# Optimization experiments

Hardware: AMD Instinct MI355X
Metric: run time of the kernel (lower is better)

Reference implementation:

```python
import jax, jax.numpy as jnp
from jax import lax
import numpy as np

B, T, D, H, O, L = 64, 1024, 256, 512, 256, 2


def setup_inputs() -> dict:
    key = jax.random.key(0)
    ks = jax.random.split(key, 12)
    s_in = 1.0 / np.sqrt(H)
    inp = {
        "x": jax.random.normal(ks[0], (B, T, D), dtype=jnp.float32),
        "W_ih0": jax.random.uniform(ks[1], (H, D), jnp.float32, -s_in, s_in),
        "W_hh0": jax.random.uniform(ks[2], (H, H), jnp.float32, -s_in, s_in),
        "b_ih0": jax.random.uniform(ks[3], (H,), jnp.float32, -s_in, s_in),
        "b_hh0": jax.random.uniform(ks[4], (H,), jnp.float32, -s_in, s_in),
        "W_ih1": jax.random.uniform(ks[5], (H, H), jnp.float32, -s_in, s_in),
        "W_hh1": jax.random.uniform(ks[6], (H, H), jnp.float32, -s_in, s_in),
        "b_ih1": jax.random.uniform(ks[7], (H,), jnp.float32, -s_in, s_in),
        "b_hh1": jax.random.uniform(ks[8], (H,), jnp.float32, -s_in, s_in),
        "W_fc": jax.random.uniform(ks[9], (O, H), jnp.float32, -s_in, s_in),
        "b_fc": jax.random.uniform(ks[10], (O,), jnp.float32, -s_in, s_in),
    }
    return inp


def _rnn_layer(inp, W_ih, W_hh, b_ih, b_hh):
    # inp: [B, T, Din] -> outputs [B, T, H], final hidden [B, H]
    # PyTorch: h_t = tanh(x_t @ W_ih^T + b_ih + h_{t-1} @ W_hh^T + b_hh)
    xW = jnp.einsum("btd,hd->bth", inp, W_ih) + b_ih + b_hh  # precompute input proj

    def step(h, xw_t):
        h = jnp.tanh(xw_t + h @ W_hh.T)
        return h, h

    h0 = jnp.zeros((inp.shape[0], W_hh.shape[0]), dtype=inp.dtype)
    hT, hs = lax.scan(step, h0, jnp.swapaxes(xW, 0, 1))  # scan over time
    return jnp.swapaxes(hs, 0, 1), hT


def reference(x, W_ih0, W_hh0, b_ih0, b_hh0, W_ih1, W_hh1, b_ih1, b_hh1, W_fc, b_fc):
    out0, _ = _rnn_layer(x, W_ih0, W_hh0, b_ih0, b_hh0)
    _, hT1 = _rnn_layer(out0, W_ih1, W_hh1, b_ih1, b_hh1)
    # fc applied to hn[-1] (last layer final hidden state)
    return hT1 @ W_fc.T + b_fc  # [B, O]
```

## Files before the change

kernel.cpp:

```cpp
#include <hip/hip_runtime.h>
#include <cmath>


#define Bdim 64
#define Tdim 1024
#define Ddim 256
#define Hdim 512
#define Odim 256

template <int K>
__global__ __launch_bounds__(1024) void gemm_rows(const float* A, const float* W,
                                                  const float* __restrict__ bias_a,
                                                  const float* __restrict__ bias_b,
                                                  float* C) {
  constexpr int KT = 16;
  __shared__ __align__(16) float As[64][KT];
  __shared__ __align__(16) float Ws[KT][516];
  const int t = threadIdx.x;
  const size_t row0 = (size_t)blockIdx.x * 64;
  const int tn = t & 127;
  const int tm = t >> 7;

  float acc[8][4];
#pragma unroll
  for (int i = 0; i < 8; ++i)
#pragma unroll
    for (int j = 0; j < 4; ++j) acc[i][j] = 0.f;

  const int r_st = t >> 4;
  const int k_st = t & 15;

  for (int k0 = 0; k0 < K; k0 += KT) {
    As[r_st][k_st] = A[(row0 + r_st) * K + k0 + k_st];
#pragma unroll
    for (int rep = 0; rep < 8; ++rep) {
      const int idx = rep * 1024 + t;
      const int n = idx >> 4;
      const int kk = idx & 15;
      Ws[kk][n] = W[(size_t)n * K + k0 + kk];
    }
    __syncthreads();
#pragma unroll
    for (int kk = 0; kk < KT; ++kk) {
      float a[8];
#pragma unroll
      for (int i = 0; i < 8; ++i) a[i] = As[tm * 8 + i][kk];
      const float4 w = *(const float4*)&Ws[kk][tn * 4];
#pragma unroll
      for (int i = 0; i < 8; ++i) {
        acc[i][0] = fmaf(a[i], w.x, acc[i][0]);
        acc[i][1] = fmaf(a[i], w.y, acc[i][1]);
        acc[i][2] = fmaf(a[i], w.z, acc[i][2]);
        acc[i][3] = fmaf(a[i], w.w, acc[i][3]);
      }
    }
    __syncthreads();
  }
  float bn[4];
#pragma unroll
  for (int j = 0; j < 4; ++j) bn[j] = bias_a[tn * 4 + j] + bias_b[tn * 4 + j];
#pragma unroll
  for (int i = 0; i < 8; ++i) {
    float4 v;
    v.x = acc[i][0] + bn[0];
    v.y = acc[i][1] + bn[1];
    v.z = acc[i][2] + bn[2];
    v.w = acc[i][3] + bn[3];
    *(float4*)&C[(row0 + tm * 8 + i) * (size_t)Hdim + tn * 4] = v;
  }
}

__global__ __launch_bounds__(512, 2) void rnn_scan_coop(
    float* xw,
    const float* __restrict__ Whh,
    unsigned long long* hbuf,
    float* h_final,
    const int store_seq) {
  const int bi = blockIdx.x;
  const int b = bi & 63;
  const int q = bi >> 6;
  const int t = threadIdx.x;
  const int ks = t >> 6;
  const int jp = t & 63;
  const int jl0 = jp * 2;
  const int jg0 = q * 128 + jl0;

  __shared__ __align__(16) float h_s[Hdim];
  __shared__ __align__(16) float red[8][128];

  float4 W0[16], W1[16];
  {
    const float4* w0p = (const float4*)(Whh + (size_t)jg0 * Hdim + ks * 64);
    const float4* w1p = (const float4*)(Whh + (size_t)(jg0 + 1) * Hdim + ks * 64);
#pragma unroll
    for (int c = 0; c < 16; ++c) {
      W0[c] = w0p[c];
      W1[c] = w1p[c];
    }
  }
#pragma unroll
  for (int c = 0; c < 16; ++c) {
    asm volatile("" : "+v"(W0[c].x), "+v"(W0[c].y), "+v"(W0[c].z), "+v"(W0[c].w));
    asm volatile("" : "+v"(W1[c].x), "+v"(W1[c].y), "+v"(W1[c].z), "+v"(W1[c].w));
  }

  h_s[t] = 0.0f;
  __syncthreads();

  float* row = xw + (size_t)b * Tdim * Hdim;

  for (int s = 0; s < Tdim; ++s, row += Hdim) {
    float xv = 0.f;
    if (t < 128) xv = row[q * 128 + t];

    const float4* h4 = (const float4*)h_s + ks * 16;
    float a0 = 0.f, a0b = 0.f, a1 = 0.f, a1b = 0.f;
#pragma unroll
    for (int c = 0; c < 16; ++c) {
      const float4 hv = h4[c];
      a0  = fmaf(W0[c].x, hv.x, a0);
      a0b = fmaf(W0[c].y, hv.y, a0b);
      a0  = fmaf(W0[c].z, hv.z, a0);
      a0b = fmaf(W0[c].w, hv.w, a0b);
      a1  = fmaf(W1[c].x, hv.x, a1);
      a1b = fmaf(W1[c].y, hv.y, a1b);
      a1  = fmaf(W1[c].z, hv.z, a1);
      a1b = fmaf(W1[c].w, hv.w, a1b);
    }
    *(float2*)&red[ks][jl0] = make_float2(a0 + a0b, a1 + a1b);
    __syncthreads();

    unsigned long long* hbW =
        hbuf + (size_t)((s + 1) & 1) * Bdim * Hdim + b * Hdim;

    if (t < 128) {
      float y = xv;
#pragma unroll
      for (int s8 = 0; s8 < 8; ++s8) y += red[s8][t];
      const float hn = tanhf(y);
      const unsigned long long pv =
          ((unsigned long long)(unsigned)(s + 1) << 32) |
          (unsigned long long)__float_as_uint(hn);
      __hip_atomic_store(&hbW[q * 128 + t], pv, __ATOMIC_RELAXED,
                         __HIP_MEMORY_SCOPE_AGENT);
      h_s[q * 128 + t] = hn;
      if (store_seq) row[q * 128 + t] = hn;
    } else {
      const int idx = t - 128;
      const int pq = idx >> 7;
      const int i = idx & 127;
      const int q2 = pq + (pq >= q);
      const unsigned long long* src = &hbW[q2 * 128 + i];
      unsigned long long v;
      do {
        v = __hip_atomic_load(src, __ATOMIC_RELAXED, __HIP_MEMORY_SCOPE_AGENT);
      } while ((unsigned)(v >> 32) != (unsigned)(s + 1));
      h_s[q2 * 128 + i] = __uint_as_float((unsigned)v);
    }
    __syncthreads();
  }

  if (h_final != nullptr && t < 128)
    h_final[(size_t)b * Hdim + q * 128 + t] = h_s[q * 128 + t];
}

__global__ __launch_bounds__(256) void fc_kernel(const float* __restrict__ h,
                                                 const float* __restrict__ Wfc,
                                                 const float* __restrict__ bfc,
                                                 float* __restrict__ out) {
  __shared__ float hs[Hdim];
  const int b = blockIdx.x, o = threadIdx.x;
  hs[o] = h[(size_t)b * Hdim + o];
  hs[o + 256] = h[(size_t)b * Hdim + 256 + o];
  __syncthreads();
  float acc = bfc[o];
  const float* wr = Wfc + (size_t)o * Hdim;
#pragma unroll 4
  for (int k = 0; k < Hdim; k += 4) {
    const float4 w = *(const float4*)(wr + k);
    acc = fmaf(w.x, hs[k], acc);
    acc = fmaf(w.y, hs[k + 1], acc);
    acc = fmaf(w.z, hs[k + 2], acc);
    acc = fmaf(w.w, hs[k + 3], acc);
  }
  out[(size_t)b * Odim + o] = acc;
}

extern "C" void kernel_launch(void* const* d_in, const int* in_sizes, int n_in,
                              void* d_out, int out_size, void* d_ws, size_t ws_size,
                              hipStream_t stream) {
  const float* x = (const float*)d_in[0];
  const float* W_ih0 = (const float*)d_in[1];
  const float* W_hh0 = (const float*)d_in[2];
  const float* b_ih0 = (const float*)d_in[3];
  const float* b_hh0 = (const float*)d_in[4];
  const float* W_ih1 = (const float*)d_in[5];
  const float* W_hh1 = (const float*)d_in[6];
  const float* b_ih1 = (const float*)d_in[7];
  const float* b_hh1 = (const float*)d_in[8];
  const float* W_fc = (const float*)d_in[9];
  const float* b_fc = (const float*)d_in[10];
  float* out = (float*)d_out;

  float* A = (float*)d_ws;
  unsigned long long* hbuf0 =
      (unsigned long long*)(A + (size_t)Bdim * Tdim * Hdim);
  unsigned long long* hbuf1 = hbuf0 + (size_t)2 * Bdim * Hdim;
  float* hT1 = (float*)(hbuf1 + (size_t)2 * Bdim * Hdim);

  gemm_rows<Ddim><<<(Bdim * Tdim) / 64, 1024, 0, stream>>>(x, W_ih0, b_ih0, b_hh0, A);

  {
    float* xwp = A;
    const float* W = W_hh0;
    unsigned long long* hb = hbuf0;
    float* hf = nullptr;
    int ss = 1;
    void* args[] = {&xwp, (void*)&W, &hb, &hf, &ss};
    hipLaunchCooperativeKernel((void*)rnn_scan_coop, dim3(Bdim * 4), dim3(512),
                               args, 0, stream);
  }

  gemm_rows<Hdim><<<(Bdim * Tdim) / 64, 1024, 0, stream>>>(A, W_ih1, b_ih1, b_hh1, A);

  {
    float* xwp = A;
    const float* W = W_hh1;
    unsigned long long* hb = hbuf1;
    float* hf = hT1;
    int ss = 0;
    void* args[] = {&xwp, (void*)&W, &hb, &hf, &ss};
    hipLaunchCooperativeKernel((void*)rnn_scan_coop, dim3(Bdim * 4), dim3(512),
                               args, 0, stream);
  }

  fc_kernel<<<Bdim, Odim, 0, stream>>>(hT1, W_fc, b_fc, out);
}
```

Baseline: 3.754 ms.

## Replace second barrier with per-wave flag polling and double-buffered hidden state

Each wave now fetches only the slice of the hidden state it consumes, polling the global tagged buffer for remote slices. For the block's own slice it spins on a workgroup-scope shared-memory sequence flag, so one of the two block-wide barriers per timestep is removed. The hidden-state and reduction buffers are double-buffered by step parity so the next step's writes cannot clobber data still being read. The next input projection is prefetched after the tanh, and the final hidden state is written directly. This shortens the per-step critical path of the serial scan, at the cost of subtler memory-ordering reasoning and spin-waiting in LDS.

```diff
diff --git a/kernel.cpp b/kernel.cpp
--- a/kernel.cpp
+++ b/kernel.cpp
@@ -80,18 +80,20 @@
   const int b = bi & 63;
   const int q = bi >> 6;
   const int t = threadIdx.x;
-  const int ks = t >> 6;
-  const int jp = t & 63;
-  const int jl0 = jp * 2;
-  const int jg0 = q * 128 + jl0;
-
-  __shared__ __align__(16) float h_s[Hdim];
-  __shared__ __align__(16) float red[8][128];
+  const int w = t >> 6;
+  const int l = t & 63;
+  const int kq = w >> 1;
+  const int half = w & 1;
+  const int jg0 = q * 128 + 2 * l;
+
+  __shared__ __align__(16) float hL[2][Hdim];
+  __shared__ __align__(16) float red[2][8][128];
+  __shared__ int ownseq[2];
 
   float4 W0[16], W1[16];
   {
-    const float4* w0p = (const float4*)(Whh + (size_t)jg0 * Hdim + ks * 64);
-    const float4* w1p = (const float4*)(Whh + (size_t)(jg0 + 1) * Hdim + ks * 64);
+    const float4* w0p = (const float4*)(Whh + (size_t)jg0 * Hdim + w * 64);
+    const float4* w1p = (const float4*)(Whh + (size_t)(jg0 + 1) * Hdim + w * 64);
 #pragma unroll
     for (int c = 0; c < 16; ++c) {
       W0[c] = w0p[c];
@@ -104,16 +106,33 @@
     asm volatile("" : "+v"(W1[c].x), "+v"(W1[c].y), "+v"(W1[c].z), "+v"(W1[c].w));
   }
 
-  h_s[t] = 0.0f;
+  hL[0][t] = 0.0f;
+  if (t < 2) ownseq[t] = 0;
   __syncthreads();
 
   float* row = xw + (size_t)b * Tdim * Hdim;
+  float xv = (t < 128) ? row[q * 128 + t] : 0.f;
 
   for (int s = 0; s < Tdim; ++s, row += Hdim) {
-    float xv = 0.f;
-    if (t < 128) xv = row[q * 128 + t];
-
-    const float4* h4 = (const float4*)h_s + ks * 16;
+    const int sp = s & 1;
+
+    if (s > 0) {
+      if (kq == q) {
+        while (__hip_atomic_load(&ownseq[half], __ATOMIC_ACQUIRE,
+                                 __HIP_MEMORY_SCOPE_WORKGROUP) < s) {
+        }
+      } else {
+        const unsigned long long* src = hbuf +
+                                        (size_t)((s - 1) & 1) * (Bdim * Hdim) +
+                                        b * Hdim + kq * 128 + half * 64 + l;
+        unsigned long long v;
+        do {
+          v = __hip_atomic_load(src, __ATOMIC_RELAXED, __HIP_MEMORY_SCOPE_AGENT);
+        } while ((unsigned)(v >> 32) != (unsigned)s);
+        hL[sp][w * 64 + l] = __uint_as_float((unsigned)v);
+      }
+    }
+    const float4* h4 = (const float4*)&hL[sp][w * 64];
     float a0 = 0.f, a0b = 0.f, a1 = 0.f, a1b = 0.f;
 #pragma unroll
     for (int c = 0; c < 16; ++c) {
@@ -127,41 +146,30 @@
       a1  = fmaf(W1[c].z, hv.z, a1);
       a1b = fmaf(W1[c].w, hv.w, a1b);
     }
-    *(float2*)&red[ks][jl0] = make_float2(a0 + a0b, a1 + a1b);
+    *(float2*)&red[sp][w][2 * l] = make_float2(a0 + a0b, a1 + a1b);
     __syncthreads();
-
-    unsigned long long* hbW =
-        hbuf + (size_t)((s + 1) & 1) * Bdim * Hdim + b * Hdim;
 
     if (t < 128) {
       float y = xv;
 #pragma unroll
-      for (int s8 = 0; s8 < 8; ++s8) y += red[s8][t];
+      for (int w8 = 0; w8 < 8; ++w8) y += red[sp][w8][t];
       const float hn = tanhf(y);
       const unsigned long long pv =
           ((unsigned long long)(unsigned)(s + 1) << 32) |
           (unsigned long long)__float_as_uint(hn);
-      __hip_atomic_store(&hbW[q * 128 + t], pv, __ATOMIC_RELAXED,
-                         __HIP_MEMORY_SCOPE_AGENT);
-      h_s[q * 128 + t] = hn;
+      __hip_atomic_store(&hbuf[(size_t)sp * (Bdim * Hdim) + b * Hdim + q * 128 + t],
+                         pv, __ATOMIC_RELAXED, __HIP_MEMORY_SCOPE_AGENT);
+      hL[sp ^ 1][q * 128 + t] = hn;
+      if (l == 0)
+        __hip_atomic_store(&ownseq[t >> 6], s + 1, __ATOMIC_RELEASE,
+                           __HIP_MEMORY_SCOPE_WORKGROUP);
       if (store_seq) row[q * 128 + t] = hn;
-    } else {
-      const int idx = t - 128;
-      const int pq = idx >> 7;
-      const int i = idx & 127;
-      const int q2 = pq + (pq >= q);
-      const unsigned long long* src = &hbW[q2 * 128 + i];
-      unsigned long long v;
-      do {
-        v = __hip_atomic_load(src, __ATOMIC_RELAXED, __HIP_MEMORY_SCOPE_AGENT);
-      } while ((unsigned)(v >> 32) != (unsigned)(s + 1));
-      h_s[q2 * 128 + i] = __uint_as_float((unsigned)v);
-    }
-    __syncthreads();
-  }
-
-  if (h_final != nullptr && t < 128)
-    h_final[(size_t)b * Hdim + q * 128 + t] = h_s[q * 128 + t];
+      if (s + 1 < Tdim)
+        xv = row[Hdim + q * 128 + t];
+      else if (h_final != nullptr)
+        h_final[(size_t)b * Hdim + q * 128 + t] = hn;
+    }
+  }
 }
 
 __global__ __launch_bounds__(256) void fc_kernel(const float* __restrict__ h,
```

Result: faster. 3.621 ms (-3.5%).
